# Performance work log

Hardware: AMD Instinct MI355X
Metric: run time of the kernel (lower is better)

The kernel has to match this reference:

```python
import jax, jax.numpy as jnp
import numpy as np

N = 50000
E = 800000
NODE_DIM = 15
HID = 64
HEADS = 4
NEG_SLOPE = 0.2


def _add_self_loops(edge_index, n):
    loops = jnp.arange(n, dtype=edge_index.dtype)
    src = jnp.concatenate([edge_index[0], loops])
    dst = jnp.concatenate([edge_index[1], loops])
    return src, dst


def gat_conv(x, edge_index, W, att_src, att_dst, bias, concat):
    # x: [N, F_in]; W: [F_in, heads*out]; att_*: [heads, out]; bias: [heads*out] or [out]
    n = x.shape[0]
    heads, out_dim = att_src.shape
    src, dst = _add_self_loops(edge_index, n)
    h = (x @ W).reshape(n, heads, out_dim)              # [N, H, D]
    a_src = jnp.sum(h * att_src[None], axis=-1)          # [N, H]
    a_dst = jnp.sum(h * att_dst[None], axis=-1)          # [N, H]
    e = a_src[src] + a_dst[dst]                          # [E', H]
    e = jnp.where(e > 0, e, NEG_SLOPE * e)               # LeakyReLU(0.2)
    # segment softmax over incoming edges of each dst node
    m = jax.ops.segment_max(e, dst, num_segments=n)      # [N, H]
    m = jnp.where(jnp.isfinite(m), m, 0.0)
    w = jnp.exp(e - m[dst])                              # [E', H]
    z = jax.ops.segment_sum(w, dst, num_segments=n)      # [N, H]
    alpha = w / z[dst]                                   # [E', H]
    msg = alpha[:, :, None] * h[src]                     # [E', H, D]
    out = jax.ops.segment_sum(msg, dst, num_segments=n)  # [N, H, D]
    if concat:
        return out.reshape(n, heads * out_dim) + bias
    return out.mean(axis=1) + bias


def setup_inputs() -> dict:
    key = jax.random.key(0)
    ks = jax.random.split(key, 11)
    x = jax.random.normal(ks[0], (N, NODE_DIM), dtype=jnp.float32)
    edge_index = jax.random.randint(ks[1], (2, E), 0, N, dtype=jnp.int64)
    s1 = 1.0 / np.sqrt(NODE_DIM)
    s2 = 1.0 / np.sqrt(HEADS * HID)
    return {
        "x": x,
        "edge_index": edge_index,
        "W1": jax.random.normal(ks[2], (NODE_DIM, HEADS * HID), dtype=jnp.float32) * s1,
        "att_src1": jax.random.normal(ks[3], (HEADS, HID), dtype=jnp.float32) * s2,
        "att_dst1": jax.random.normal(ks[4], (HEADS, HID), dtype=jnp.float32) * s2,
        "b1": jnp.zeros((HEADS * HID,), dtype=jnp.float32),
        "W2": jax.random.normal(ks[5], (HEADS * HID, HID), dtype=jnp.float32) * s2,
        "att_src2": jax.random.normal(ks[6], (1, HID), dtype=jnp.float32) * s2,
        "att_dst2": jax.random.normal(ks[7], (1, HID), dtype=jnp.float32) * s2,
        "b2": jnp.zeros((HID,), dtype=jnp.float32),
    }


def reference(x, edge_index, W1, att_src1, att_dst1, b1, W2, att_src2, att_dst2, b2):
    h = gat_conv(x, edge_index, W1, att_src1, att_dst1, b1, concat=True)   # [N, 256]
    h = jax.nn.elu(h)
    # dropout p=0.2 skipped (eval mode)
    h = gat_conv(h, edge_index, W2, att_src2, att_dst2, b2, concat=True)   # heads=1 -> [N, 64]
    return h.mean(axis=0)                                                   # [64]
```

## Files before the change

### kernel.cpp

```cpp
#include <hip/hip_runtime.h>
#include <hip/hip_fp16.h>

#define NNODES 50000
#define NEDGES 800000
#define NEG_SLOPE 0.2f
#define NTOT (NEDGES + NNODES)
#define NB_NODE ((NNODES + 255) / 256)
#define CHUNK 4096
#define NCHUNK ((NEDGES + CHUNK - 1) / CHUNK)
#define CAPB 4800
#define CNTSTRIDE 16

typedef _Float16 half8 __attribute__((ext_vector_type(8)));
typedef _Float16 half4 __attribute__((ext_vector_type(4)));
typedef float f32x4 __attribute__((ext_vector_type(4)));

__global__ void setup_scatter(const float* __restrict__ x, const float* __restrict__ W1,
                              const float* __restrict__ att_src, const float* __restrict__ att_dst,
                              const float* __restrict__ W2,
                              const int* __restrict__ srcs, const int* __restrict__ dsts,
                              int* __restrict__ bucket_cnt, int* __restrict__ bucketbuf,
                              float* __restrict__ x16, float* __restrict__ asrc4,
                              float* __restrict__ adst4, _Float16* __restrict__ W2T) {
    int t = threadIdx.x;
    __shared__ unsigned short meta[CHUNK];
    __shared__ int lcnt[NB_NODE], lbase[NB_NODE];
    __shared__ float swa[16][4], swd[16][4];
    if (blockIdx.x < NCHUNK) {
        int b = blockIdx.x;
        for (int i = t; i < NB_NODE; i += 256) lcnt[i] = 0;
        __syncthreads();
        int e0 = b * CHUNK;
        int e1 = e0 + CHUNK; if (e1 > NEDGES) e1 = NEDGES;
        for (int e = e0 + t; e < e1; e += 256) {
            int d = dsts[e];
            meta[e - e0] = (unsigned short)d;
            atomicAdd(&lcnt[d >> 8], 1);
        }
        __syncthreads();
        for (int i = t; i < NB_NODE; i += 256) {
            int c = lcnt[i];
            lbase[i] = c ? atomicAdd(&bucket_cnt[i * CNTSTRIDE], c) : 0;
        }
        __syncthreads();
        for (int i = t; i < NB_NODE; i += 256) lcnt[i] = 0;
        __syncthreads();
        for (int e = e0 + t; e < e1; e += 256) {
            int dv = meta[e - e0];
            int bk = dv >> 8;
            int pos = lbase[bk] + atomicAdd(&lcnt[bk], 1);
            if (pos < CAPB) bucketbuf[bk * CAPB + pos] = ((dv & 255) << 16) | srcs[e];
        }
    } else {
        int b = blockIdx.x - NCHUNK;
        if (t < 128) {
            int k = (t & 63) >> 2, h = t & 3;
            float s = 0.f;
            if (k < 15) {
                const float* att = (t < 64) ? att_src : att_dst;
#pragma unroll 16
                for (int d = 0; d < 64; ++d)
                    s += W1[k * 256 + h * 64 + d] * att[h * 64 + d];
            }
            if (t < 64) swa[k][h] = s; else swd[k][h] = s;
        }
        int tid = b * 256 + t;
        if (tid < 64 * 256) {
            int n = tid >> 8, k = tid & 255;
            W2T[n * 256 + k] = (_Float16)W2[k * 64 + n];
        }
        __syncthreads();
        int nid = tid;
        if (nid < NNODES) {
            float xv[16];
#pragma unroll
            for (int k = 0; k < 15; ++k) xv[k] = x[nid * 15 + k];
            xv[15] = 0.f;
#pragma unroll
            for (int k = 0; k < 16; k += 4)
                *(float4*)(x16 + (size_t)nid * 16 + k) =
                    make_float4(xv[k], xv[k+1], xv[k+2], xv[k+3]);
            float ps[4] = {0.f, 0.f, 0.f, 0.f}, pd[4] = {0.f, 0.f, 0.f, 0.f};
#pragma unroll
            for (int k = 0; k < 15; ++k)
#pragma unroll
                for (int h = 0; h < 4; ++h) {
                    ps[h] += xv[k] * swa[k][h];
                    pd[h] += xv[k] * swd[k][h];
                }
            *(float4*)(asrc4 + nid * 4) = make_float4(ps[0], ps[1], ps[2], ps[3]);
            *(float4*)(adst4 + nid * 4) = make_float4(pd[0], pd[1], pd[2], pd[3]);
        }
    }
}

__global__ void scanA(const int* __restrict__ bucket_cnt, const int* __restrict__ bucketbuf,
                      int* __restrict__ rowstart, int* __restrict__ partials) {
    int b = blockIdx.x, t = threadIdx.x, lane = t & 63, wid = t >> 6;
    __shared__ int hist[256];
    __shared__ int ws[4];
    int i = b * 256 + t;
    hist[t] = (i < NNODES) ? 1 : 0;
    __syncthreads();
    int n = bucket_cnt[b * CNTSTRIDE]; if (n > CAPB) n = CAPB;
    const int* buf = bucketbuf + (size_t)b * CAPB;
    for (int j = t; j < n; j += 256)
        atomicAdd(&hist[buf[j] >> 16], 1);
    __syncthreads();
    int v = (i < NNODES) ? hist[t] : 0;
    int incl = v;
#pragma unroll
    for (int off = 1; off < 64; off <<= 1) {
        int u = __shfl_up(incl, off, 64);
        if (lane >= off) incl += u;
    }
    if (lane == 63) ws[wid] = incl;
    __syncthreads();
    int w0 = ws[0], w1 = ws[1], w2 = ws[2], w3 = ws[3];
    int woff = (wid > 0 ? w0 : 0) + (wid > 1 ? w1 : 0) + (wid > 2 ? w2 : 0);
    if (i < NNODES) rowstart[i] = woff + (incl - v);
    if (t == 0) partials[b] = w0 + w1 + w2 + w3;
}

__global__ void scanB(const int* __restrict__ partials, int* __restrict__ blockoff,
                      int* __restrict__ rowstart, int nb) {
    int t = threadIdx.x, lane = t & 63, wid = t >> 6;
    int v = (t < nb) ? partials[t] : 0;
    int incl = v;
#pragma unroll
    for (int off = 1; off < 64; off <<= 1) {
        int u = __shfl_up(incl, off, 64);
        if (lane >= off) incl += u;
    }
    __shared__ int ws[4];
    if (lane == 63) ws[wid] = incl;
    __syncthreads();
    int w0 = ws[0], w1 = ws[1], w2 = ws[2], w3 = ws[3];
    int woff = (wid > 0 ? w0 : 0) + (wid > 1 ? w1 : 0) + (wid > 2 ? w2 : 0);
    if (t < nb) blockoff[t] = woff + (incl - v);
    if (t == 0) rowstart[NNODES] = w0 + w1 + w2 + w3;
}

__global__ void scanC(int* __restrict__ rowstart, const int* __restrict__ blockoff) {
    int b = blockIdx.x, t = threadIdx.x;
    int i = b * 256 + t;
    if (i < NNODES) rowstart[i] += blockoff[b];
}

__global__ void local_sort(const int* __restrict__ bucket_cnt, const int* __restrict__ bucketbuf,
                           const int* __restrict__ rowstart,
                           const float4* __restrict__ asrc4, const float4* __restrict__ adst4,
                           int* __restrict__ srclist, float4* __restrict__ sw4) {
    int b = blockIdx.x, t = threadIdx.x;
    __shared__ int cur[256];
    __shared__ int local[8192];
    __shared__ float4 sadst[256];
    int idx = b * 256 + t; if (idx > NNODES) idx = NNODES;
    int base = rowstart[b * 256];
    cur[t] = rowstart[idx] - base;
    int nid = b * 256 + t;
    if (nid < NNODES) sadst[t] = adst4[nid];
    __syncthreads();
    if (nid < NNODES) {
        int pos = atomicAdd(&cur[t], 1);
        local[pos] = (t << 16) | nid;
    }
    int n = bucket_cnt[b * CNTSTRIDE]; if (n > CAPB) n = CAPB;
    const int* buf = bucketbuf + (size_t)b * CAPB;
    for (int i = t; i < n; i += 256) {
        int entry = buf[i];
        int pos = atomicAdd(&cur[entry >> 16], 1);
        local[pos] = entry;
    }
    __syncthreads();
    int endidx = (b + 1) * 256; if (endidx > NNODES) endidx = NNODES;
    int total = rowstart[endidx] - base;
    for (int i = t; i < total; i += 256) {
        int e = local[i];
        int s = e & 0xFFFF, dl = e >> 16;
        srclist[base + i] = s;
        float4 as = asrc4[s];
        float4 ad = sadst[dl];
        float e0 = as.x + ad.x, e1 = as.y + ad.y, e2 = as.z + ad.z, e3 = as.w + ad.w;
        e0 = fmaxf(e0, NEG_SLOPE * e0); e1 = fmaxf(e1, NEG_SLOPE * e1);
        e2 = fmaxf(e2, NEG_SLOPE * e2); e3 = fmaxf(e3, NEG_SLOPE * e3);
        sw4[base + i] = make_float4(__expf(e0), __expf(e1), __expf(e2), __expf(e3));
    }
}

__global__ void layer1_aggr(const float* __restrict__ x16, const int* __restrict__ rowstart,
                            const int* __restrict__ srclist, const float* __restrict__ sw4,
                            const float* __restrict__ W1, const float* __restrict__ b1,
                            __half* __restrict__ out1) {
    int wid = threadIdx.x >> 6, lane = threadIdx.x & 63;
    int nid = blockIdx.x * 4 + wid;
    int h = lane >> 4, k = lane & 15;
    int beg = __builtin_amdgcn_readfirstlane(rowstart[nid]);
    int end = __builtin_amdgcn_readfirstlane(rowstart[nid + 1]);
    float acc = 0.f, zs = 0.f;
    int i0 = beg;
    int nfull = beg + ((end - beg) & ~3);
    for (; i0 < nfull; i0 += 4) {
        int s0 = __builtin_amdgcn_readfirstlane(srclist[i0]);
        int s1 = __builtin_amdgcn_readfirstlane(srclist[i0 + 1]);
        int s2 = __builtin_amdgcn_readfirstlane(srclist[i0 + 2]);
        int s3 = __builtin_amdgcn_readfirstlane(srclist[i0 + 3]);
        float w0 = sw4[(i0 + 0) * 4 + h];
        float w1 = sw4[(i0 + 1) * 4 + h];
        float w2 = sw4[(i0 + 2) * 4 + h];
        float w3 = sw4[(i0 + 3) * 4 + h];
        float xv0 = x16[s0 * 16 + k];
        float xv1 = x16[s1 * 16 + k];
        float xv2 = x16[s2 * 16 + k];
        float xv3 = x16[s3 * 16 + k];
        zs += (w0 + w1) + (w2 + w3);
        acc = fmaf(w0, xv0, acc);
        acc = fmaf(w1, xv1, acc);
        acc = fmaf(w2, xv2, acc);
        acc = fmaf(w3, xv3, acc);
    }
    for (; i0 < end; ++i0) {
        int s = __builtin_amdgcn_readfirstlane(srclist[i0]);
        float w = sw4[i0 * 4 + h];
        zs += w;
        acc = fmaf(w, x16[s * 16 + k], acc);
    }
    __shared__ float sacc[4][64];
    sacc[wid][lane] = acc * (1.f / zs);
    int c = lane, h2 = c >> 4;
    float o0 = 0.f, o1 = 0.f, o2 = 0.f, o3 = 0.f;
#pragma unroll
    for (int kk = 0; kk < 15; ++kk) {
        float a = sacc[wid][h2 * 16 + kk];
        float4 wv = *(const float4*)(W1 + kk * 256 + c * 4);
        o0 = fmaf(a, wv.x, o0); o1 = fmaf(a, wv.y, o1);
        o2 = fmaf(a, wv.z, o2); o3 = fmaf(a, wv.w, o3);
    }
    float4 bo = *(const float4*)(b1 + c * 4);
    o0 += bo.x; o1 += bo.y; o2 += bo.z; o3 += bo.w;
    o0 = o0 > 0.f ? o0 : __expf(o0) - 1.f;
    o1 = o1 > 0.f ? o1 : __expf(o1) - 1.f;
    o2 = o2 > 0.f ? o2 : __expf(o2) - 1.f;
    o3 = o3 > 0.f ? o3 : __expf(o3) - 1.f;
    half4 st;
    st[0] = (_Float16)o0; st[1] = (_Float16)o1; st[2] = (_Float16)o2; st[3] = (_Float16)o3;
    *(half4*)((_Float16*)out1 + (size_t)nid * 256 + c * 4) = st;
}


__global__ __launch_bounds__(256) void layer2_gemm(const __half* __restrict__ out1,
                                                   const _Float16* __restrict__ W2T,
                                                   __half* __restrict__ h2,
                                                   const float* __restrict__ att_src2,
                                                   const float* __restrict__ att_dst2,
                                                   float* __restrict__ as2,
                                                   float* __restrict__ ad2) {
    int w = threadIdx.x >> 6, lane = threadIdx.x & 63;
    int m16 = lane & 15, quad = lane >> 4;
    int r0 = blockIdx.x * 64 + w * 16;
    const _Float16* A = (const _Float16*)out1;
    f32x4 acc[4] = {{0.f,0.f,0.f,0.f},{0.f,0.f,0.f,0.f},{0.f,0.f,0.f,0.f},{0.f,0.f,0.f,0.f}};
    int row = r0 + m16; if (row >= NNODES) row = NNODES - 1;
#pragma unroll
    for (int k0 = 0; k0 < 256; k0 += 32) {
        half8 a = *(const half8*)(A + (size_t)row * 256 + k0 + quad * 8);
#pragma unroll
        for (int nt = 0; nt < 4; ++nt) {
            half8 b = *(const half8*)(W2T + (size_t)(nt * 16 + m16) * 256 + k0 + quad * 8);
            acc[nt] = __builtin_amdgcn_mfma_f32_16x16x32_f16(a, b, acc[nt], 0, 0, 0);
        }
    }
    __shared__ _Float16 tile[64][72];
#pragma unroll
    for (int nt = 0; nt < 4; ++nt)
#pragma unroll
        for (int r = 0; r < 4; ++r)
            tile[w * 16 + quad * 4 + r][nt * 16 + m16] = (_Float16)acc[nt][r];
    __syncthreads();
    int t = threadIdx.x;
    int trow = t >> 2, seg = t & 3;
    int rg = blockIdx.x * 64 + trow;
    if (rg < NNODES) {
        float4 v0 = *(float4*)&tile[trow][seg * 16];
        float4 v1 = *(float4*)&tile[trow][seg * 16 + 8];
        _Float16* dst = (_Float16*)h2 + (size_t)rg * 64 + seg * 16;
        *(float4*)dst = v0;
        *(float4*)(dst + 8) = v1;
        const _Float16* hv = &tile[trow][seg * 16];
        float ps = 0.f, pd = 0.f;
#pragma unroll
        for (int j = 0; j < 16; ++j) {
            float v = (float)hv[j];
            ps += v * att_src2[seg * 16 + j];
            pd += v * att_dst2[seg * 16 + j];
        }
        ps += __shfl_xor(ps, 1, 64); ps += __shfl_xor(ps, 2, 64);
        pd += __shfl_xor(pd, 1, 64); pd += __shfl_xor(pd, 2, 64);
        if (seg == 0) { as2[rg] = ps; ad2[rg] = pd; }
    }
}

__global__ void layer2_aggr(const __half* __restrict__ h2, const int* __restrict__ rowstart,
                            const int* __restrict__ srclist,
                            const float* __restrict__ as2, const float* __restrict__ ad2,
                            const float* __restrict__ b2, float* __restrict__ out2) {
    int wid = threadIdx.x >> 6, lane = threadIdx.x & 63;
    int nid = blockIdx.x * 4 + wid;
    int q = lane >> 4, c = lane & 15;
    int beg = __builtin_amdgcn_readfirstlane(rowstart[nid]);
    int end = __builtin_amdgcn_readfirstlane(rowstart[nid + 1]);
    float ad = ad2[nid];
    const __half* hb = h2 + c * 4;
    __half2 z16 = __float2half2_rn(0.f);
    __half2 acc0 = z16, acc1 = z16;
    float zs = 0.f;
    for (int i0 = beg; i0 < end; i0 += 16) {
#pragma unroll
        for (int u = 0; u < 4; ++u) {
            int i = i0 + q + 4 * u;
            bool valid = i < end;
            int s = valid ? srclist[i] : 0;
            float2 gv = *(const float2*)(hb + (size_t)s * 64);
            float e = as2[s] + ad;
            e = fmaxf(e, NEG_SLOPE * e);
            float w = valid ? __expf(e) : 0.f;
            zs += w;
            __half2 wh = __float2half2_rn(w);
            acc0 = __hfma2(wh, *(__half2*)&gv.x, acc0);
            acc1 = __hfma2(wh, *(__half2*)&gv.y, acc1);
        }
    }
    float2 f0 = __half22float2(acc0), f1 = __half22float2(acc1);
    float ax = f0.x, ay = f0.y, az = f1.x, aw = f1.y;
#pragma unroll
    for (int off = 16; off < 64; off <<= 1) {
        ax += __shfl_xor(ax, off, 64);
        ay += __shfl_xor(ay, off, 64);
        az += __shfl_xor(az, off, 64);
        aw += __shfl_xor(aw, off, 64);
        zs += __shfl_xor(zs, off, 64);
    }
    if (lane < 16) {
        float rz = 1.f / zs;
        float4 bo = ((const float4*)b2)[c];
        float4 st = make_float4(ax * rz + bo.x, ay * rz + bo.y,
                                az * rz + bo.z, aw * rz + bo.w);
        *(float4*)(out2 + (size_t)nid * 64 + c * 4) = st;
    }
}


__global__ void reduce_kernel(const float* __restrict__ out2, float* __restrict__ dout) {
    int t = threadIdx.x;
    int col = t & 63, sub = t >> 6;
    float acc = 0.f;
    for (int r = blockIdx.x * 4 + sub; r < NNODES; r += 256 * 4)
        acc += out2[r * 64 + col];
    __shared__ float sh[256];
    sh[t] = acc;
    __syncthreads();
    if (t < 64) {
        float v = sh[t] + sh[t + 64] + sh[t + 128] + sh[t + 192];
        atomicAdd(&dout[t], v * (1.0f / NNODES));
    }
}


extern "C" void kernel_launch(void* const* d_in, const int* in_sizes, int n_in,
                              void* d_out, int out_size, void* d_ws, size_t ws_size,
                              hipStream_t stream) {
    const float* x        = (const float*)d_in[0];
    const int*   ei       = (const int*)d_in[1];
    const float* W1       = (const float*)d_in[2];
    const float* att_src1 = (const float*)d_in[3];
    const float* att_dst1 = (const float*)d_in[4];
    const float* b1       = (const float*)d_in[5];
    const float* W2       = (const float*)d_in[6];
    const float* att_src2 = (const float*)d_in[7];
    const float* att_dst2 = (const float*)d_in[8];
    const float* b2       = (const float*)d_in[9];
    float* out = (float*)d_out;

    char* ws = (char*)d_ws;
    size_t off = 0;
    auto take = [&](size_t bytes) -> char* {
        char* p = ws + off;
        off = (off + bytes + 255) & ~(size_t)255;
        return p;
    };
    int*      bucket_cnt = (int*)take((size_t)NB_NODE * CNTSTRIDE * sizeof(int));
    int*      bucketbuf  = (int*)take((size_t)NB_NODE * CAPB * sizeof(int));
    int*      rowstart   = (int*)take((NNODES + 1) * sizeof(int));
    int*      partials   = (int*)take(256 * sizeof(int));
    int*      blockoff   = (int*)take(256 * sizeof(int));
    int*      srclist    = (int*)take(((size_t)NTOT + 16) * sizeof(int));
    float*    sw4        = (float*)take(((size_t)NTOT + 16) * 4 * sizeof(float));
    float*    x16        = (float*)take((size_t)NNODES * 16 * sizeof(float));
    float*    asrc4      = (float*)take((size_t)NNODES * 4 * sizeof(float));
    float*    adst4      = (float*)take((size_t)NNODES * 4 * sizeof(float));
    __half*   out1       = (__half*)take((size_t)NNODES * 256 * sizeof(__half));
    _Float16* W2T        = (_Float16*)take(64 * 256 * sizeof(_Float16));
    __half*   h2         = (__half*)take((size_t)NNODES * 64 * sizeof(__half));
    float*    as2        = (float*)take((size_t)NNODES * sizeof(float));
    float*    ad2        = (float*)take((size_t)NNODES * sizeof(float));
    float*    out2       = (float*)take((size_t)NNODES * 64 * sizeof(float));

    const int* srcs = ei;
    const int* dsts = ei + NEDGES;

    hipMemsetAsync(d_out, 0, 64 * sizeof(float), stream);
    hipMemsetAsync(bucket_cnt, 0, (size_t)NB_NODE * CNTSTRIDE * sizeof(int), stream);

    setup_scatter<<<NCHUNK + NB_NODE, 256, 0, stream>>>(x, W1, att_src1, att_dst1, W2,
                                                        srcs, dsts, bucket_cnt, bucketbuf,
                                                        x16, asrc4, adst4, W2T);
    scanA<<<NB_NODE, 256, 0, stream>>>(bucket_cnt, bucketbuf, rowstart, partials);
    scanB<<<1, 256, 0, stream>>>(partials, blockoff, rowstart, NB_NODE);
    scanC<<<NB_NODE, 256, 0, stream>>>(rowstart, blockoff);
    local_sort<<<NB_NODE, 256, 0, stream>>>(bucket_cnt, bucketbuf, rowstart,
                                            (const float4*)asrc4, (const float4*)adst4,
                                            srclist, (float4*)sw4);

    layer1_aggr<<<NNODES / 4, 256, 0, stream>>>(x16, rowstart, srclist, sw4, W1, b1, out1);

    layer2_gemm<<<(NNODES + 63) / 64, 256, 0, stream>>>(out1, W2T, h2, att_src2, att_dst2,
                                                        as2, ad2);
    layer2_aggr<<<NNODES / 4, 256, 0, stream>>>(h2, rowstart, srclist, as2, ad2, b2, out2);

    reduce_kernel<<<256, 256, 0, stream>>>(out2, out);
}
```

Before: 228.6 us.

## Fuse scan fixup into local_sort and batch-load source indices per wave

Removes the scanC kernel by applying block offsets inside local_sort and using partials for the bucket total. Layer1 and layer2 aggregation now load up to 64 source indices per wave in one coalesced read and broadcast them with readlane, instead of issuing scalar loads per edge. Layer2 switches from four edges at a time per quarter-wave with fp16 accumulation to one edge per iteration across the full 64 lanes with fp32 accumulation, which drops the cross-lane reduction. The cost is more serial iterations per node in layer2 and reliance on partials holding the per-block edge count.

```diff
diff --git a/kernel.cpp b/kernel.cpp
--- a/kernel.cpp
+++ b/kernel.cpp
@@ -141,26 +141,24 @@
     if (t == 0) rowstart[NNODES] = w0 + w1 + w2 + w3;
 }
 
-__global__ void scanC(int* __restrict__ rowstart, const int* __restrict__ blockoff) {
-    int b = blockIdx.x, t = threadIdx.x;
-    int i = b * 256 + t;
-    if (i < NNODES) rowstart[i] += blockoff[b];
-}
-
 __global__ void local_sort(const int* __restrict__ bucket_cnt, const int* __restrict__ bucketbuf,
-                           const int* __restrict__ rowstart,
+                           int* __restrict__ rowstart, const int* __restrict__ blockoff,
+                           const int* __restrict__ partials,
                            const float4* __restrict__ asrc4, const float4* __restrict__ adst4,
                            int* __restrict__ srclist, float4* __restrict__ sw4) {
     int b = blockIdx.x, t = threadIdx.x;
     __shared__ int cur[256];
     __shared__ int local[8192];
     __shared__ float4 sadst[256];
-    int idx = b * 256 + t; if (idx > NNODES) idx = NNODES;
-    int base = rowstart[b * 256];
-    cur[t] = rowstart[idx] - base;
-    int nid = b * 256 + t;
+    int boff = blockoff[b];
+    int base = rowstart[b * 256] + boff;
+    int idx = b * 256 + t;
+    int fin = (idx < NNODES) ? rowstart[idx] + boff : 0;
+    cur[t] = (idx < NNODES) ? (fin - base) : 0;
+    int nid = idx;
     if (nid < NNODES) sadst[t] = adst4[nid];
     __syncthreads();
+    if (nid < NNODES) rowstart[nid] = fin;
     if (nid < NNODES) {
         int pos = atomicAdd(&cur[t], 1);
         local[pos] = (t << 16) | nid;
@@ -173,8 +171,7 @@
         local[pos] = entry;
     }
     __syncthreads();
-    int endidx = (b + 1) * 256; if (endidx > NNODES) endidx = NNODES;
-    int total = rowstart[endidx] - base;
+    int total = partials[b];
     for (int i = t; i < total; i += 256) {
         int e = local[i];
         int s = e & 0xFFFF, dl = e >> 16;
@@ -197,33 +194,28 @@
     int h = lane >> 4, k = lane & 15;
     int beg = __builtin_amdgcn_readfirstlane(rowstart[nid]);
     int end = __builtin_amdgcn_readfirstlane(rowstart[nid + 1]);
+    int cnt = end - beg;
     float acc = 0.f, zs = 0.f;
-    int i0 = beg;
-    int nfull = beg + ((end - beg) & ~3);
-    for (; i0 < nfull; i0 += 4) {
-        int s0 = __builtin_amdgcn_readfirstlane(srclist[i0]);
-        int s1 = __builtin_amdgcn_readfirstlane(srclist[i0 + 1]);
-        int s2 = __builtin_amdgcn_readfirstlane(srclist[i0 + 2]);
-        int s3 = __builtin_amdgcn_readfirstlane(srclist[i0 + 3]);
-        float w0 = sw4[(i0 + 0) * 4 + h];
-        float w1 = sw4[(i0 + 1) * 4 + h];
-        float w2 = sw4[(i0 + 2) * 4 + h];
-        float w3 = sw4[(i0 + 3) * 4 + h];
-        float xv0 = x16[s0 * 16 + k];
-        float xv1 = x16[s1 * 16 + k];
-        float xv2 = x16[s2 * 16 + k];
-        float xv3 = x16[s3 * 16 + k];
-        zs += (w0 + w1) + (w2 + w3);
-        acc = fmaf(w0, xv0, acc);
-        acc = fmaf(w1, xv1, acc);
-        acc = fmaf(w2, xv2, acc);
-        acc = fmaf(w3, xv3, acc);
-    }
-    for (; i0 < end; ++i0) {
-        int s = __builtin_amdgcn_readfirstlane(srclist[i0]);
-        float w = sw4[i0 * 4 + h];
-        zs += w;
-        acc = fmaf(w, x16[s * 16 + k], acc);
+    for (int c0 = 0; c0 < cnt; c0 += 64) {
+        int rem = cnt - c0; if (rem > 64) rem = 64;
+        int sv = (c0 + lane < cnt) ? srclist[beg + c0 + lane] : 0;
+        int j = 0;
+        for (; j + 8 <= rem; j += 8) {
+#pragma unroll
+            for (int u = 0; u < 8; ++u) {
+                int s = __builtin_amdgcn_readlane(sv, j + u);
+                float w = sw4[(size_t)(beg + c0 + j + u) * 4 + h];
+                float xv = x16[s * 16 + k];
+                zs += w;
+                acc = fmaf(w, xv, acc);
+            }
+        }
+        for (; j < rem; ++j) {
+            int s = __builtin_amdgcn_readlane(sv, j);
+            float w = sw4[(size_t)(beg + c0 + j) * 4 + h];
+            zs += w;
+            acc = fmaf(w, x16[s * 16 + k], acc);
+        }
     }
     __shared__ float sacc[4][64];
     sacc[wid][lane] = acc * (1.f / zs);
@@ -306,47 +298,37 @@
                             const float* __restrict__ b2, float* __restrict__ out2) {
     int wid = threadIdx.x >> 6, lane = threadIdx.x & 63;
     int nid = blockIdx.x * 4 + wid;
-    int q = lane >> 4, c = lane & 15;
     int beg = __builtin_amdgcn_readfirstlane(rowstart[nid]);
     int end = __builtin_amdgcn_readfirstlane(rowstart[nid + 1]);
+    int cnt = end - beg;
     float ad = ad2[nid];
-    const __half* hb = h2 + c * 4;
-    __half2 z16 = __float2half2_rn(0.f);
-    __half2 acc0 = z16, acc1 = z16;
-    float zs = 0.f;
-    for (int i0 = beg; i0 < end; i0 += 16) {
-#pragma unroll
-        for (int u = 0; u < 4; ++u) {
-            int i = i0 + q + 4 * u;
-            bool valid = i < end;
-            int s = valid ? srclist[i] : 0;
-            float2 gv = *(const float2*)(hb + (size_t)s * 64);
+    float acc = 0.f, zs = 0.f;
+    for (int c0 = 0; c0 < cnt; c0 += 64) {
+        int rem = cnt - c0; if (rem > 64) rem = 64;
+        int sv = (c0 + lane < cnt) ? srclist[beg + c0 + lane] : 0;
+        int j = 0;
+        for (; j + 8 <= rem; j += 8) {
+#pragma unroll
+            for (int u = 0; u < 8; ++u) {
+                int s = __builtin_amdgcn_readlane(sv, j + u);
+                float e = as2[s] + ad;
+                e = fmaxf(e, NEG_SLOPE * e);
+                float w = __expf(e);
+                float xv = __half2float(h2[(size_t)s * 64 + lane]);
+                zs += w;
+                acc = fmaf(w, xv, acc);
+            }
+        }
+        for (; j < rem; ++j) {
+            int s = __builtin_amdgcn_readlane(sv, j);
             float e = as2[s] + ad;
             e = fmaxf(e, NEG_SLOPE * e);
-            float w = valid ? __expf(e) : 0.f;
+            float w = __expf(e);
             zs += w;
-            __half2 wh = __float2half2_rn(w);
-            acc0 = __hfma2(wh, *(__half2*)&gv.x, acc0);
-            acc1 = __hfma2(wh, *(__half2*)&gv.y, acc1);
-        }
-    }
-    float2 f0 = __half22float2(acc0), f1 = __half22float2(acc1);
-    float ax = f0.x, ay = f0.y, az = f1.x, aw = f1.y;
-#pragma unroll
-    for (int off = 16; off < 64; off <<= 1) {
-        ax += __shfl_xor(ax, off, 64);
-        ay += __shfl_xor(ay, off, 64);
-        az += __shfl_xor(az, off, 64);
-        aw += __shfl_xor(aw, off, 64);
-        zs += __shfl_xor(zs, off, 64);
-    }
-    if (lane < 16) {
-        float rz = 1.f / zs;
-        float4 bo = ((const float4*)b2)[c];
-        float4 st = make_float4(ax * rz + bo.x, ay * rz + bo.y,
-                                az * rz + bo.z, aw * rz + bo.w);
-        *(float4*)(out2 + (size_t)nid * 64 + c * 4) = st;
-    }
+            acc = fmaf(w, __half2float(h2[(size_t)s * 64 + lane]), acc);
+        }
+    }
+    out2[(size_t)nid * 64 + lane] = acc / zs + b2[lane];
 }
 
 
@@ -393,8 +375,8 @@
     int*      rowstart   = (int*)take((NNODES + 1) * sizeof(int));
     int*      partials   = (int*)take(256 * sizeof(int));
     int*      blockoff   = (int*)take(256 * sizeof(int));
-    int*      srclist    = (int*)take(((size_t)NTOT + 16) * sizeof(int));
-    float*    sw4        = (float*)take(((size_t)NTOT + 16) * 4 * sizeof(float));
+    int*      srclist    = (int*)take(((size_t)NTOT + 64) * sizeof(int));
+    float*    sw4        = (float*)take(((size_t)NTOT + 64) * 4 * sizeof(float));
     float*    x16        = (float*)take((size_t)NNODES * 16 * sizeof(float));
     float*    asrc4      = (float*)take((size_t)NNODES * 4 * sizeof(float));
     float*    adst4      = (float*)take((size_t)NNODES * 4 * sizeof(float));
@@ -416,8 +398,7 @@
                                                         x16, asrc4, adst4, W2T);
     scanA<<<NB_NODE, 256, 0, stream>>>(bucket_cnt, bucketbuf, rowstart, partials);
     scanB<<<1, 256, 0, stream>>>(partials, blockoff, rowstart, NB_NODE);
-    scanC<<<NB_NODE, 256, 0, stream>>>(rowstart, blockoff);
-    local_sort<<<NB_NODE, 256, 0, stream>>>(bucket_cnt, bucketbuf, rowstart,
+    local_sort<<<NB_NODE, 256, 0, stream>>>(bucket_cnt, bucketbuf, rowstart, blockoff, partials,
                                             (const float4*)asrc4, (const float4*)adst4,
                                             srclist, (float4*)sw4);
 
```

Result: slower. 234.2 us (+2.4%).
